# Kernel optimization log

Hardware: AMD Instinct MI355X
Metric: run time of the kernel (lower is better)

## Reference

```python
import jax, jax.numpy as jnp
import numpy as np
import math

B, T, D, H = 4, 2048, 1024, 16
HD = D // H  # head dim = 64
ROPE_BASE = 10000.0


def apply_rope(x):
    # x: [b, h, t, hd]. Positions start at 1 (seq_id = arange(1, t+1)) per the source.
    t, hd = x.shape[2], x.shape[3]
    half = hd // 2
    theta = 1.0 / (ROPE_BASE ** (jnp.arange(0, hd, 2, dtype=jnp.float32) / hd))  # [hd/2]
    pos = jnp.arange(1, t + 1, dtype=jnp.float32)  # [t]
    ang = pos[:, None] * theta[None, :]             # [t, hd/2]
    ang = jnp.concatenate([ang, ang], axis=-1)      # [t, hd]
    sin, cos = jnp.sin(ang), jnp.cos(ang)
    # rotate-half: cat([-x2, x1])
    rot = jnp.concatenate([-x[..., half:], x[..., :half]], axis=-1)
    return x * cos[None, None, :, :] + rot * sin[None, None, :, :]


def setup_inputs() -> dict:
    key = jax.random.key(0)
    ks = jax.random.split(key, 9)
    s = 1.0 / math.sqrt(D)
    return {
        "x": jax.random.normal(ks[0], (B, T, D), dtype=jnp.float32),
        "Wq": jax.random.normal(ks[1], (D, D), dtype=jnp.float32) * s,
        "bq": jax.random.normal(ks[2], (D,), dtype=jnp.float32) * 0.01,
        "Wk": jax.random.normal(ks[3], (D, D), dtype=jnp.float32) * s,
        "bk": jax.random.normal(ks[4], (D,), dtype=jnp.float32) * 0.01,
        "Wv": jax.random.normal(ks[5], (D, D), dtype=jnp.float32) * s,
        "bv": jax.random.normal(ks[6], (D,), dtype=jnp.float32) * 0.01,
        "Wo": jax.random.normal(ks[7], (D, D), dtype=jnp.float32) * s,
        "bo": jax.random.normal(ks[8], (D,), dtype=jnp.float32) * 0.01,
    }


def reference(x, Wq, bq, Wk, bk, Wv, bv, Wo, bo):
    b, t, d = x.shape
    h, hd = H, HD
    # projections (torch Linear: x @ W.T + b)
    q = x @ Wq.T + bq
    k = x @ Wk.T + bk
    v = x @ Wv.T + bv
    # [b, t, d] -> [b, h, t, hd]
    split = lambda z: z.reshape(b, t, h, hd).transpose(0, 2, 1, 3)
    q, k, v = split(q), split(k), split(v)
    q = apply_rope(q)
    k = apply_rope(k)
    scale = math.sqrt(hd)
    att = jnp.einsum('bhqd,bhkd->bhqk', q, k) / scale
    mask = jnp.tril(jnp.ones((t, t), dtype=bool))
    att = jnp.where(mask[None, None, :, :], att, -jnp.inf)
    att = jax.nn.softmax(att, axis=-1)
    y = jnp.einsum('bhqk,bhkd->bhqd', att, v)
    y = y.transpose(0, 2, 1, 3).reshape(b, t, d)
    y = y @ Wo.T + bo
    return y
```

## Files before the change

kernel.cpp:

```cpp
#include <hip/hip_runtime.h>

#define BB 4
#define TT 2048
#define DD 1024
#define HH 16
#define HD 64

typedef __attribute__((ext_vector_type(8))) _Float16 f16x8;
typedef __attribute__((ext_vector_type(4))) float f32x4;
typedef __attribute__((ext_vector_type(2))) unsigned int u32x2;
typedef __attribute__((ext_vector_type(4))) unsigned int u32x4;

__device__ __forceinline__ float h2f(unsigned short u) {
    return (float)__builtin_bit_cast(_Float16, u);
}
__device__ __forceinline__ unsigned short f2h(float f) {
    return __builtin_bit_cast(unsigned short, (_Float16)f);
}
__device__ __forceinline__ unsigned int pkrtz(float a, float b) {
    return __builtin_bit_cast(unsigned int, __builtin_amdgcn_cvt_pkrtz(a, b));
}

__global__ __launch_bounds__(256) void conv_all(
    const float4* __restrict__ x,
    const float4* __restrict__ Wq, const float4* __restrict__ Wk,
    const float4* __restrict__ Wv,
    ushort4* __restrict__ xh, ushort4* __restrict__ wh,
    float2* __restrict__ tab)
{
    int vi = blockIdx.x * 256 + threadIdx.x;
    if (vi < 2097152) {
        float4 v = x[vi];
        xh[vi] = (ushort4){ f2h(v.x), f2h(v.y), f2h(v.z), f2h(v.w) };
    } else if (vi < 2883584) {
        int u = vi - 2097152;
        int w = u >> 18;
        const float4* src = (w == 0) ? Wq : (w == 1) ? Wk : Wv;
        float4 v = src[u & 262143];
        wh[u] = (ushort4){ f2h(v.x), f2h(v.y), f2h(v.z), f2h(v.w) };
    } else {
        int u = vi - 2883584;
        int t = u >> 5, i = u & 31;
        float ang = (float)(t + 1) *
                    exp2f(-(float)i * (13.287712379549449f / 32.0f));
        tab[u] = (float2){ cosf(ang), sinf(ang) };
    }
}

__global__ __launch_bounds__(256) void conv_wo(
    const float4* __restrict__ Wo, ushort4* __restrict__ dst)
{
    int i = blockIdx.x * 256 + threadIdx.x;
    float4 v = Wo[i];
    dst[i] = (ushort4){ f2h(v.x), f2h(v.y), f2h(v.z), f2h(v.w) };
}

__global__ __launch_bounds__(256) void gemm_qkv(
    const unsigned short* __restrict__ A,
    const unsigned short* __restrict__ Wall,
    const float* __restrict__ bq, const float* __restrict__ bk,
    const float* __restrict__ bv,
    const float2* __restrict__ tab,
    unsigned short* __restrict__ qkv)
{
    __shared__ __align__(16) unsigned short As[128 * 64];
    __shared__ __align__(16) unsigned short Ws[128 * 64];

    int bid = blockIdx.x;
    int swz = (bid & 7) * 192 + (bid >> 3);
    int bx = swz % 24, by = swz / 24;
    const int sel = bx >> 3;
    const int jb = bx & 7;
    const int n0 = by * 128;
    const int j0 = jb * 128;

    const unsigned short* W = Wall + (size_t)sel * 1048576;
    const float* bias = (sel == 0) ? bq : (sel == 1) ? bk : bv;
    unsigned short* outp = qkv + (size_t)sel * (BB * HH * TT * HD);

    const int tid = threadIdx.x;
    const int w = tid >> 6, lane = tid & 63;
    const int l15 = lane & 15, g = lane >> 4;
    const int wr = w >> 1, wc = w & 1;

    f32x4 acc[4][4];
#pragma unroll
    for (int mi = 0; mi < 4; mi++)
#pragma unroll
        for (int nj = 0; nj < 4; nj++) acc[mi][nj] = (f32x4){0.f, 0.f, 0.f, 0.f};

    u32x4 pa[4], pb[4];
#define LOADREGS(KS)                                                             \
    {                                                                            \
        _Pragma("unroll")                                                        \
        for (int it = 0; it < 4; it++) {                                         \
            int ci = tid + it * 256;                                             \
            int r = ci >> 3, p = ci & 7;                                         \
            pa[it] = *(const u32x4*)(A + (size_t)(n0 + r) * 1024 + (KS) + p * 8);\
            pb[it] = *(const u32x4*)(W + (size_t)(j0 + r) * 1024 + (KS) + p * 8);\
        }                                                                        \
    }

    LOADREGS(0)

    for (int ks = 0; ks < 1024; ks += 64) {
        __syncthreads();
#pragma unroll
        for (int it = 0; it < 4; it++) {
            int ci = tid + it * 256;
            int r = ci >> 3, p = ci & 7;
            int d = r * 64 + ((p ^ (r & 7)) << 3);
            *(u32x4*)(As + d) = pa[it];
            *(u32x4*)(Ws + d) = pb[it];
        }
        __syncthreads();
        if (ks + 64 < 1024) LOADREGS(ks + 64)

#pragma unroll
        for (int c = 0; c < 2; c++) {
            f16x8 af[4], bf[4];
            const int q0c = c * 4 + (g >> 1);
            const int q1c = q0c + 2;
            const int off = (g & 1) << 2;
#pragma unroll
            for (int mi = 0; mi < 4; mi++) {
                int r = wr * 64 + mi * 16 + l15;
                int sw = r & 7;
                const unsigned short* rp = As + r * 64;
                u32x2 x0 = *(const u32x2*)(rp + ((q0c ^ sw) << 3) + off);
                u32x2 x1 = *(const u32x2*)(rp + ((q1c ^ sw) << 3) + off);
                u32x4 uu = {x0.x, x0.y, x1.x, x1.y};
                af[mi] = __builtin_bit_cast(f16x8, uu);
            }
#pragma unroll
            for (int nj = 0; nj < 4; nj++) {
                int r = wc * 64 + nj * 16 + l15;
                int sw = r & 7;
                const unsigned short* rp = Ws + r * 64;
                u32x2 x0 = *(const u32x2*)(rp + ((q0c ^ sw) << 3) + off);
                u32x2 x1 = *(const u32x2*)(rp + ((q1c ^ sw) << 3) + off);
                u32x4 uu = {x0.x, x0.y, x1.x, x1.y};
                bf[nj] = __builtin_bit_cast(f16x8, uu);
            }
#pragma unroll
            for (int mi = 0; mi < 4; mi++)
#pragma unroll
                for (int nj = 0; nj < 4; nj++)
                    acc[mi][nj] = __builtin_amdgcn_mfma_f32_16x16x32_f16(
                        af[mi], bf[nj], acc[mi][nj], 0, 0, 0);
        }
    }
#undef LOADREGS

    float bb4[4];
#pragma unroll
    for (int nj = 0; nj < 4; nj++) bb4[nj] = bias[j0 + wc * 64 + nj * 16 + l15];
    const int hh = (j0 >> 6) + wc;

    if (sel == 2) {
#pragma unroll
        for (int mi = 0; mi < 4; mi++)
#pragma unroll
            for (int r = 0; r < 4; r++) {
                int n = n0 + wr * 64 + mi * 16 + 4 * g + r;
                int b = n >> 11, t = n & (TT - 1);
                size_t rowbase = ((size_t)(b * HH + hh) * TT + t) << 6;
#pragma unroll
                for (int nj = 0; nj < 4; nj++) {
                    int dd = nj * 16 + l15;
                    outp[rowbase + dd] = f2h(acc[mi][nj][r] + bb4[nj]);
                }
            }
    } else {
#pragma unroll
        for (int mi = 0; mi < 4; mi++)
#pragma unroll
            for (int r = 0; r < 4; r++) {
                int n = n0 + wr * 64 + mi * 16 + 4 * g + r;
                int b = n >> 11, t = n & (TT - 1);
                size_t rowbase = ((size_t)(b * HH + hh) * TT + t) << 6;
                const float2* tp = tab + t * 32 + l15;
#pragma unroll
                for (int p = 0; p < 2; p++) {
                    float2 cs = tp[p * 16];
                    float x1 = acc[mi][p][r]     + bb4[p];
                    float x2 = acc[mi][p + 2][r] + bb4[p + 2];
                    int i = p * 16 + l15;
                    outp[rowbase + i]      = f2h(x1 * cs.x - x2 * cs.y);
                    outp[rowbase + i + 32] = f2h(x2 * cs.x + x1 * cs.y);
                }
            }
    }
}

__global__ __launch_bounds__(256) void gemm_h(
    const unsigned short* __restrict__ A, const unsigned short* __restrict__ W,
    const float* __restrict__ bias, float* __restrict__ outp,
    int N, int K, int J)
{
    __shared__ __align__(16) unsigned short As[128 * 64];
    __shared__ __align__(16) unsigned short Ws[128 * 64];

    int total = gridDim.x * gridDim.y;
    int flat = blockIdx.y * gridDim.x + blockIdx.x;
    int swz = (flat & 7) * (total >> 3) + (flat >> 3);
    int bxi = swz % gridDim.x, byi = swz / gridDim.x;

    const int tid = threadIdx.x;
    const int w = tid >> 6, lane = tid & 63;
    const int l15 = lane & 15, g = lane >> 4;
    const int wr = w >> 1, wc = w & 1;
    const int n0 = byi * 128;
    const int j0 = bxi * 128;

    f32x4 acc[4][4];
#pragma unroll
    for (int mi = 0; mi < 4; mi++)
#pragma unroll
        for (int nj = 0; nj < 4; nj++) acc[mi][nj] = (f32x4){0.f, 0.f, 0.f, 0.f};

    u32x4 pa[4], pb[4];
#define LOADREGS(KS)                                                          \
    {                                                                         \
        _Pragma("unroll")                                                     \
        for (int it = 0; it < 4; it++) {                                      \
            int ci = tid + it * 256;                                          \
            int r = ci >> 3, p = ci & 7;                                      \
            pa[it] = *(const u32x4*)(A + (size_t)(n0 + r) * K + (KS) + p * 8);\
            pb[it] = *(const u32x4*)(W + (size_t)(j0 + r) * K + (KS) + p * 8);\
        }                                                                     \
    }

    LOADREGS(0)

    for (int ks = 0; ks < K; ks += 64) {
        __syncthreads();
#pragma unroll
        for (int it = 0; it < 4; it++) {
            int ci = tid + it * 256;
            int r = ci >> 3, p = ci & 7;
            int d = r * 64 + ((p ^ (r & 7)) << 3);
            *(u32x4*)(As + d) = pa[it];
            *(u32x4*)(Ws + d) = pb[it];
        }
        __syncthreads();
        if (ks + 64 < K) LOADREGS(ks + 64)

#pragma unroll
        for (int c = 0; c < 2; c++) {
            f16x8 af[4], bf[4];
            const int q0c = c * 4 + (g >> 1);
            const int q1c = q0c + 2;
            const int off = (g & 1) << 2;
#pragma unroll
            for (int mi = 0; mi < 4; mi++) {
                int r = wr * 64 + mi * 16 + l15;
                int sw = r & 7;
                const unsigned short* rp = As + r * 64;
                u32x2 x0 = *(const u32x2*)(rp + ((q0c ^ sw) << 3) + off);
                u32x2 x1 = *(const u32x2*)(rp + ((q1c ^ sw) << 3) + off);
                u32x4 uu = {x0.x, x0.y, x1.x, x1.y};
                af[mi] = __builtin_bit_cast(f16x8, uu);
            }
#pragma unroll
            for (int nj = 0; nj < 4; nj++) {
                int r = wc * 64 + nj * 16 + l15;
                int sw = r & 7;
                const unsigned short* rp = Ws + r * 64;
                u32x2 x0 = *(const u32x2*)(rp + ((q0c ^ sw) << 3) + off);
                u32x2 x1 = *(const u32x2*)(rp + ((q1c ^ sw) << 3) + off);
                u32x4 uu = {x0.x, x0.y, x1.x, x1.y};
                bf[nj] = __builtin_bit_cast(f16x8, uu);
            }
#pragma unroll
            for (int mi = 0; mi < 4; mi++)
#pragma unroll
                for (int nj = 0; nj < 4; nj++)
                    acc[mi][nj] = __builtin_amdgcn_mfma_f32_16x16x32_f16(
                        af[mi], bf[nj], acc[mi][nj], 0, 0, 0);
        }
    }
#undef LOADREGS

#pragma unroll
    for (int nj = 0; nj < 4; nj++) {
        int j = j0 + wc * 64 + nj * 16 + l15;
        float bb = bias[j];
#pragma unroll
        for (int mi = 0; mi < 4; mi++)
#pragma unroll
            for (int r = 0; r < 4; r++) {
                int n = n0 + wr * 64 + mi * 16 + 4 * g + r;
                outp[(size_t)n * J + j] = acc[mi][nj][r] + bb;
            }
    }
}

__device__ __forceinline__ u32x2 ds_tr16(const unsigned short* p) {
    u32x2 r;
    asm volatile("ds_read_b64_tr_b16 %0, %1"
                 : "=v"(r)
                 : "v"((unsigned int)(unsigned long long)p));
    return r;
}

__global__ __launch_bounds__(512, 4) void attn_mfma(
    const unsigned short* __restrict__ q,
    const unsigned short* __restrict__ k,
    const unsigned short* __restrict__ v,
    unsigned short* __restrict__ aout)
{
    __shared__ __align__(16) unsigned short Ks[64 * 64];
    __shared__ __align__(16) unsigned short Vs[4 * 1056];

    const int h = blockIdx.y, b = blockIdx.z;
    const int tid = threadIdx.x;
    const int w = tid >> 6;
    const int wd = w & 3;
    const int wt = w >> 2;
    const int lane = tid & 63;
    const int l15 = lane & 15, g = lane >> 4;
    const int bh = b * HH + h;
    const size_t base = (size_t)bh * TT * 64;
    const unsigned short* Qp = q + base;
    const unsigned short* Kp = k + base;
    const unsigned short* Vp = v + base;

    const float SC = 0.18033688011112042f;

    u32x4 kreg;
    u32x2 vreg[2];
#define LOADKV(KB)                                                             \
    {                                                                          \
        {                                                                      \
            int key = tid >> 3, pr = tid & 7;                                  \
            kreg = *(const u32x4*)(Kp + (size_t)((KB) + key) * 64 + pr * 8);   \
        }                                                                      \
        _Pragma("unroll")                                                      \
        for (int it = 0; it < 2; it++) {                                       \
            int vi = tid + it * 512;                                           \
            int key = vi >> 4, c4 = vi & 15;                                   \
            vreg[it] = *(const u32x2*)(Vp + (size_t)((KB) + key) * 64 + c4 * 4);\
        }                                                                      \
    }

    for (int ph = 0; ph < 2; ph++) {
        const int qs = ph ? (15 - (int)blockIdx.x) : (int)blockIdx.x;
        const int q0 = qs * 128;
        const int dtile = 2 * qs + wt;

        f16x8 qf[2];
        {
            const unsigned short* Qr = Qp + (size_t)(q0 + w * 16 + l15) * 64;
#pragma unroll
            for (int c = 0; c < 2; c++) {
                u32x2 a0 = *(const u32x2*)(Qr + 32 * c + 4 * g);
                u32x2 a1 = *(const u32x2*)(Qr + 32 * c + 16 + 4 * g);
                u32x4 uu = {a0.x, a0.y, a1.x, a1.y};
                qf[c] = __builtin_bit_cast(f16x8, uu);
            }
        }

        float mrow = -1e30f, lrow = 0.f;
        f32x4 accO[4];
#pragma unroll
        for (int nb = 0; nb < 4; nb++) accO[nb] = (f32x4){0.f, 0.f, 0.f, 0.f};

        const int ntiles = 2 * qs + 2;
        LOADKV(0)

        for (int kt = 0; kt < ntiles; kt++) {
            const bool active = (kt <= dtile);
            const bool diag = (kt == dtile);
            __syncthreads();
            {
                int key = tid >> 3, pr = tid & 7;
                *(u32x4*)(Ks + key * 64 + ((pr ^ (key & 7)) << 3)) = kreg;
            }
#pragma unroll
            for (int it = 0; it < 2; it++) {
                int vi = tid + it * 512;
                int key = vi >> 4, c4 = vi & 15;
                *(u32x2*)(Vs + (c4 >> 2) * 1056 + key * 16 + (c4 & 3) * 4) = vreg[it];
            }
            __syncthreads();
            if (kt + 1 < ntiles) LOADKV((kt + 1) * 64)

            if (active) {
                const int nkb = diag ? (wd + 1) : 4;
                f32x4 accS[4];
#pragma unroll
                for (int kb = 0; kb < 4; kb++) accS[kb] = (f32x4){0.f, 0.f, 0.f, 0.f};
                __builtin_amdgcn_s_setprio(1);
#pragma unroll
                for (int kb = 0; kb < 4; kb++) {
                    if (kb < nkb) {
                        int key = kb * 16 + l15;
                        int sw = key & 7;
#pragma unroll
                        for (int c = 0; c < 2; c++) {
                            int c8a = 8 * c + g, c8b = 8 * c + 4 + g;
                            u32x2 x0 = *(const u32x2*)(Ks + key * 64 +
                                           (((c8a >> 1) ^ sw) << 3) + ((c8a & 1) << 2));
                            u32x2 x1 = *(const u32x2*)(Ks + key * 64 +
                                           (((c8b >> 1) ^ sw) << 3) + ((c8b & 1) << 2));
                            u32x4 uu = {x0.x, x0.y, x1.x, x1.y};
                            accS[kb] = __builtin_amdgcn_mfma_f32_16x16x32_f16(
                                __builtin_bit_cast(f16x8, uu), qf[c], accS[kb], 0, 0, 0);
                        }
                    }
                }
                __builtin_amdgcn_s_setprio(0);

                float sloc[16];
                float tmax = -1e30f;
                if (diag) {
#pragma unroll
                    for (int kb = 0; kb < 4; kb++)
#pragma unroll
                        for (int r = 0; r < 4; r++) {
                            float s = accS[kb][r];
                            bool valid = (kb * 16 + 4 * g + r <= wd * 16 + l15);
                            s = valid ? s : -1e30f;
                            sloc[kb * 4 + r] = s;
                            tmax = fmaxf(tmax, s);
                        }
                } else {
#pragma unroll
                    for (int kb = 0; kb < 4; kb++)
#pragma unroll
                        for (int r = 0; r < 4; r++) {
                            float s = accS[kb][r];
                            sloc[kb * 4 + r] = s;
                            tmax = fmaxf(tmax, s);
                        }
                }
                tmax = fmaxf(tmax, __shfl_xor(tmax, 16));
                tmax = fmaxf(tmax, __shfl_xor(tmax, 32));

                if (!__all(tmax - mrow <= 61.0f)) {
                    float mnew = fmaxf(mrow, tmax);
                    float sf = exp2f((mrow - mnew) * SC);
                    mrow = mnew;
                    lrow *= sf;
                    float sfr[4];
#pragma unroll
                    for (int r = 0; r < 4; r++) sfr[r] = __shfl(sf, 4 * g + r);
#pragma unroll
                    for (int nb = 0; nb < 4; nb++)
#pragma unroll
                        for (int r = 0; r < 4; r++) accO[nb][r] *= sfr[r];
                }

                const float nmsc = -mrow * SC;
                unsigned int pw[8];
                float psum = 0.f;
#pragma unroll
                for (int i = 0; i < 8; i++) {
                    float p0 = exp2f(fmaf(sloc[2 * i],     SC, nmsc));
                    float p1 = exp2f(fmaf(sloc[2 * i + 1], SC, nmsc));
                    pw[i] = pkrtz(p0, p1);
                    psum += p0 + p1;
                }
                psum += __shfl_xor(psum, 16);
                psum += __shfl_xor(psum, 32);
                lrow += psum;

                const int nkc = (diag && wd < 2) ? 1 : 2;
#pragma unroll
                for (int kc = 0; kc < 2; kc++)
                    if (kc < nkc) {
                        u32x2 vfr[4][2];
#pragma unroll
                        for (int nb = 0; nb < 4; nb++)
#pragma unroll
                            for (int t2 = 0; t2 < 2; t2++)
                                vfr[nb][t2] = ds_tr16(
                                    Vs + nb * 1056 + (kc * 32 + 16 * t2) * 16 + 4 * lane);
                        asm volatile("s_waitcnt lgkmcnt(0)" ::: "memory");
                        __builtin_amdgcn_sched_barrier(0);
                        u32x4 pu = {pw[4 * kc + 0], pw[4 * kc + 1], pw[4 * kc + 2], pw[4 * kc + 3]};
                        f16x8 pf = __builtin_bit_cast(f16x8, pu);
                        __builtin_amdgcn_s_setprio(1);
#pragma unroll
                        for (int nb = 0; nb < 4; nb++) {
                            u32x4 vu = {vfr[nb][0].x, vfr[nb][0].y,
                                        vfr[nb][1].x, vfr[nb][1].y};
                            accO[nb] = __builtin_amdgcn_mfma_f32_16x16x32_f16(
                                pf, __builtin_bit_cast(f16x8, vu), accO[nb], 0, 0, 0);
                        }
                        __builtin_amdgcn_s_setprio(0);
                    }
            }
        }

        float linv = 1.0f / lrow;
        float sfr[4];
#pragma unroll
        for (int r = 0; r < 4; r++) sfr[r] = __shfl(linv, 4 * g + r);
#pragma unroll
        for (int r = 0; r < 4; r++) {
            int qr = q0 + w * 16 + 4 * g + r;
            unsigned short* orow = aout + (size_t)(b * TT + qr) * DD + h * 64;
#pragma unroll
            for (int nb = 0; nb < 4; nb++)
                orow[nb * 16 + l15] = f2h(accO[nb][r] * sfr[r]);
        }
    }
#undef LOADKV
}

extern "C" void kernel_launch(void* const* d_in, const int* in_sizes, int n_in,
                              void* d_out, int out_size, void* d_ws, size_t ws_size,
                              hipStream_t stream)
{
    const float* x  = (const float*)d_in[0];
    const float* Wq = (const float*)d_in[1];
    const float* bq = (const float*)d_in[2];
    const float* Wk = (const float*)d_in[3];
    const float* bk = (const float*)d_in[4];
    const float* Wv = (const float*)d_in[5];
    const float* bv = (const float*)d_in[6];
    const float* Wo = (const float*)d_in[7];
    const float* bo = (const float*)d_in[8];
    float* out = (float*)d_out;

    const size_t NE = (size_t)BB * HH * TT * HD;
    unsigned short* qkv  = (unsigned short*)d_ws;
    unsigned short* qb   = qkv;
    unsigned short* kbuf = qkv + NE;
    unsigned short* vbuf = qkv + 2 * NE;
    float* res = (float*)d_ws;

    unsigned short* ds  = (unsigned short*)d_out;
    unsigned short* xh  = ds;
    unsigned short* wh  = ds + 8388608;
    float2* tab = (float2*)(ds + 11534336);

    const bool direct = ws_size >= (size_t)8 * NE;
    unsigned short* att = direct ? (qkv + 3 * NE) : ds;
    unsigned short* woh = direct ? (unsigned short*)d_ws : (ds + 11796480);
    float* resout = direct ? out : res;

    const int N = BB * TT;
    dim3 blk(256);

    conv_all<<<11520, blk, 0, stream>>>(
        (const float4*)x, (const float4*)Wq, (const float4*)Wk,
        (const float4*)Wv, (ushort4*)xh, (ushort4*)wh, tab);

    gemm_qkv<<<1536, blk, 0, stream>>>(xh, wh, bq, bk, bv, tab, qkv);

    attn_mfma<<<dim3(8, HH, BB), dim3(512), 0, stream>>>(qb, kbuf, vbuf, att);

    conv_wo<<<1024, blk, 0, stream>>>((const float4*)Wo, (ushort4*)woh);

    gemm_h<<<dim3(DD / 128, N / 128), blk, 0, stream>>>(att, woh, bo, resout, N, DD, DD);

    if (!direct)
        hipMemcpyAsync(out, res, (size_t)N * DD * sizeof(float),
                       hipMemcpyDeviceToDevice, stream);
}
```

Before: 286.8 us.

## Double-buffer GEMM tiles with direct global-to-LDS loads

Both GEMM kernels (QKV projection and output projection) now load A and W tiles straight into LDS with global_load_lds instead of staging them in registers. The XOR swizzle moves from the LDS write address to the global read address. LDS is double-buffered, so the next K-tile is fetched while the current one is used, and only one barrier per iteration is needed. This frees the staging registers and drops the separate LDS store pass. In exchange, LDS use doubles to 64KB per block, which may lower occupancy, and correctness depends on the barrier waiting for the outstanding loads.

```diff
diff --git a/kernel.cpp b/kernel.cpp
--- a/kernel.cpp
+++ b/kernel.cpp
@@ -55,6 +55,11 @@
     dst[i] = (ushort4){ f2h(v.x), f2h(v.y), f2h(v.z), f2h(v.w) };
 }
 
+#define GLDS(gp, lp)                                                          \
+    __builtin_amdgcn_global_load_lds(                                         \
+        (const __attribute__((address_space(1))) unsigned int*)(gp),          \
+        (__attribute__((address_space(3))) unsigned int*)(lp), 16, 0, 0)
+
 __global__ __launch_bounds__(256) void gemm_qkv(
     const unsigned short* __restrict__ A,
     const unsigned short* __restrict__ Wall,
@@ -63,8 +68,8 @@
     const float2* __restrict__ tab,
     unsigned short* __restrict__ qkv)
 {
-    __shared__ __align__(16) unsigned short As[128 * 64];
-    __shared__ __align__(16) unsigned short Ws[128 * 64];
+    __shared__ __align__(16) unsigned short As[2 * 128 * 64];
+    __shared__ __align__(16) unsigned short Ws[2 * 128 * 64];
 
     int bid = blockIdx.x;
     int swz = (bid & 7) * 192 + (bid >> 3);
@@ -82,6 +87,7 @@
     const int w = tid >> 6, lane = tid & 63;
     const int l15 = lane & 15, g = lane >> 4;
     const int wr = w >> 1, wc = w & 1;
+    const int wavebase = tid & ~63;
 
     f32x4 acc[4][4];
 #pragma unroll
@@ -89,32 +95,27 @@
 #pragma unroll
         for (int nj = 0; nj < 4; nj++) acc[mi][nj] = (f32x4){0.f, 0.f, 0.f, 0.f};
 
-    u32x4 pa[4], pb[4];
-#define LOADREGS(KS)                                                             \
-    {                                                                            \
-        _Pragma("unroll")                                                        \
-        for (int it = 0; it < 4; it++) {                                         \
-            int ci = tid + it * 256;                                             \
-            int r = ci >> 3, p = ci & 7;                                         \
-            pa[it] = *(const u32x4*)(A + (size_t)(n0 + r) * 1024 + (KS) + p * 8);\
-            pb[it] = *(const u32x4*)(W + (size_t)(j0 + r) * 1024 + (KS) + p * 8);\
-        }                                                                        \
-    }
-
-    LOADREGS(0)
-
-    for (int ks = 0; ks < 1024; ks += 64) {
+#define ISSUE(KS, BUF)                                                        \
+    {                                                                         \
+        _Pragma("unroll")                                                     \
+        for (int it = 0; it < 4; it++) {                                      \
+            int ci = it * 256 + tid;                                          \
+            int r = ci >> 3;                                                  \
+            int p = (ci & 7) ^ (r & 7);                                       \
+            int lb = (BUF) * 8192 + (it * 256 + wavebase) * 8;                \
+            GLDS(A + (size_t)(n0 + r) * 1024 + (KS) + p * 8, As + lb);        \
+            GLDS(W + (size_t)(j0 + r) * 1024 + (KS) + p * 8, Ws + lb);        \
+        }                                                                     \
+    }
+
+    ISSUE(0, 0)
+
+    for (int ki = 0; ki < 16; ki++) {
+        const int cur = ki & 1;
         __syncthreads();
-#pragma unroll
-        for (int it = 0; it < 4; it++) {
-            int ci = tid + it * 256;
-            int r = ci >> 3, p = ci & 7;
-            int d = r * 64 + ((p ^ (r & 7)) << 3);
-            *(u32x4*)(As + d) = pa[it];
-            *(u32x4*)(Ws + d) = pb[it];
-        }
-        __syncthreads();
-        if (ks + 64 < 1024) LOADREGS(ks + 64)
+        if (ki + 1 < 16) ISSUE((ki + 1) * 64, cur ^ 1)
+        const unsigned short* Ab = As + cur * 8192;
+        const unsigned short* Wb = Ws + cur * 8192;
 
 #pragma unroll
         for (int c = 0; c < 2; c++) {
@@ -126,7 +127,7 @@
             for (int mi = 0; mi < 4; mi++) {
                 int r = wr * 64 + mi * 16 + l15;
                 int sw = r & 7;
-                const unsigned short* rp = As + r * 64;
+                const unsigned short* rp = Ab + r * 64;
                 u32x2 x0 = *(const u32x2*)(rp + ((q0c ^ sw) << 3) + off);
                 u32x2 x1 = *(const u32x2*)(rp + ((q1c ^ sw) << 3) + off);
                 u32x4 uu = {x0.x, x0.y, x1.x, x1.y};
@@ -136,7 +137,7 @@
             for (int nj = 0; nj < 4; nj++) {
                 int r = wc * 64 + nj * 16 + l15;
                 int sw = r & 7;
-                const unsigned short* rp = Ws + r * 64;
+                const unsigned short* rp = Wb + r * 64;
                 u32x2 x0 = *(const u32x2*)(rp + ((q0c ^ sw) << 3) + off);
                 u32x2 x1 = *(const u32x2*)(rp + ((q1c ^ sw) << 3) + off);
                 u32x4 uu = {x0.x, x0.y, x1.x, x1.y};
@@ -150,7 +151,7 @@
                         af[mi], bf[nj], acc[mi][nj], 0, 0, 0);
         }
     }
-#undef LOADREGS
+#undef ISSUE
 
     float bb4[4];
 #pragma unroll
@@ -198,8 +199,8 @@
     const float* __restrict__ bias, float* __restrict__ outp,
     int N, int K, int J)
 {
-    __shared__ __align__(16) unsigned short As[128 * 64];
-    __shared__ __align__(16) unsigned short Ws[128 * 64];
+    __shared__ __align__(16) unsigned short As[2 * 128 * 64];
+    __shared__ __align__(16) unsigned short Ws[2 * 128 * 64];
 
     int total = gridDim.x * gridDim.y;
     int flat = blockIdx.y * gridDim.x + blockIdx.x;
@@ -212,6 +213,7 @@
     const int wr = w >> 1, wc = w & 1;
     const int n0 = byi * 128;
     const int j0 = bxi * 128;
+    const int wavebase = tid & ~63;
 
     f32x4 acc[4][4];
 #pragma unroll
@@ -219,32 +221,28 @@
 #pragma unroll
         for (int nj = 0; nj < 4; nj++) acc[mi][nj] = (f32x4){0.f, 0.f, 0.f, 0.f};
 
-    u32x4 pa[4], pb[4];
-#define LOADREGS(KS)                                                          \
+#define ISSUE(KS, BUF)                                                        \
     {                                                                         \
         _Pragma("unroll")                                                     \
         for (int it = 0; it < 4; it++) {                                      \
-            int ci = tid + it * 256;                                          \
-            int r = ci >> 3, p = ci & 7;                                      \
-            pa[it] = *(const u32x4*)(A + (size_t)(n0 + r) * K + (KS) + p * 8);\
-            pb[it] = *(const u32x4*)(W + (size_t)(j0 + r) * K + (KS) + p * 8);\
+            int ci = it * 256 + tid;                                          \
+            int r = ci >> 3;                                                  \
+            int p = (ci & 7) ^ (r & 7);                                       \
+            int lb = (BUF) * 8192 + (it * 256 + wavebase) * 8;                \
+            GLDS(A + (size_t)(n0 + r) * K + (KS) + p * 8, As + lb);           \
+            GLDS(W + (size_t)(j0 + r) * K + (KS) + p * 8, Ws + lb);           \
         }                                                                     \
     }
 
-    LOADREGS(0)
-
-    for (int ks = 0; ks < K; ks += 64) {
+    const int nks = K >> 6;
+    ISSUE(0, 0)
+
+    for (int ki = 0; ki < nks; ki++) {
+        const int cur = ki & 1;
         __syncthreads();
-#pragma unroll
-        for (int it = 0; it < 4; it++) {
-            int ci = tid + it * 256;
-            int r = ci >> 3, p = ci & 7;
-            int d = r * 64 + ((p ^ (r & 7)) << 3);
-            *(u32x4*)(As + d) = pa[it];
-            *(u32x4*)(Ws + d) = pb[it];
-        }
-        __syncthreads();
-        if (ks + 64 < K) LOADREGS(ks + 64)
+        if (ki + 1 < nks) ISSUE((ki + 1) * 64, cur ^ 1)
+        const unsigned short* Ab = As + cur * 8192;
+        const unsigned short* Wb = Ws + cur * 8192;
 
 #pragma unroll
         for (int c = 0; c < 2; c++) {
@@ -256,7 +254,7 @@
             for (int mi = 0; mi < 4; mi++) {
                 int r = wr * 64 + mi * 16 + l15;
                 int sw = r & 7;
-                const unsigned short* rp = As + r * 64;
+                const unsigned short* rp = Ab + r * 64;
                 u32x2 x0 = *(const u32x2*)(rp + ((q0c ^ sw) << 3) + off);
                 u32x2 x1 = *(const u32x2*)(rp + ((q1c ^ sw) << 3) + off);
                 u32x4 uu = {x0.x, x0.y, x1.x, x1.y};
@@ -266,7 +264,7 @@
             for (int nj = 0; nj < 4; nj++) {
                 int r = wc * 64 + nj * 16 + l15;
                 int sw = r & 7;
-                const unsigned short* rp = Ws + r * 64;
+                const unsigned short* rp = Wb + r * 64;
                 u32x2 x0 = *(const u32x2*)(rp + ((q0c ^ sw) << 3) + off);
                 u32x2 x1 = *(const u32x2*)(rp + ((q1c ^ sw) << 3) + off);
                 u32x4 uu = {x0.x, x0.y, x1.x, x1.y};
@@ -280,7 +278,7 @@
                         af[mi], bf[nj], acc[mi][nj], 0, 0, 0);
         }
     }
-#undef LOADREGS
+#undef ISSUE
 
 #pragma unroll
     for (int nj = 0; nj < 4; nj++) {
```

New measurement: 283.9 us. Within noise of the previous version (-1.0%).
